# Kernel tuning notes

Hardware: AMD Instinct MI355X
Metric: run time of the kernel (lower is better)

Reference implementation:

```python
import jax, jax.numpy as jnp
import numpy as np
from jax import lax

EPS = 1e-5

def setup_inputs() -> dict:
    key = jax.random.key(0)
    k1, k2, k3, k4, k5, k6 = jax.random.split(key, 6)
    x = jax.random.normal(k1, (1, 64, 31, 96, 96), dtype=jnp.float32)
    # small init scale keeps gate pre-activations in a sane range
    w = jax.random.normal(k2, (256, 64, 3, 3, 3), dtype=jnp.float32) * 0.05
    gamma = jax.random.uniform(k3, (256,), dtype=jnp.float32)
    beta = jax.random.normal(k4, (256,), dtype=jnp.float32) * 0.1
    mean = jax.random.normal(k5, (256,), dtype=jnp.float32) * 0.1
    var = jax.random.uniform(k6, (256,), dtype=jnp.float32) + 0.5
    return {"x": x, "w": w, "gamma": gamma, "beta": beta, "mean": mean, "var": var}

def _bcast(p):
    return p[None, :, None, None, None]

def reference(x, w, gamma, beta, mean, var):
    # Conv3d (bias=False), stride 1, padding 1, NCDHW
    gates = lax.conv_general_dilated(
        x, w, window_strides=(1, 1, 1), padding=[(1, 1)] * 3,
        dimension_numbers=("NCDHW", "OIDHW", "NCDHW"))
    # BatchNorm3d (inference, running stats)
    scale = gamma * lax.rsqrt(var + EPS)
    gates = gates * _bcast(scale) + _bcast(beta - mean * scale)
    C = 64  # out_channels
    Wx = jnp.tanh(gates[:, 0 * C:1 * C])
    ft = jax.nn.sigmoid(gates[:, 1 * C:2 * C])
    rt = jax.nn.sigmoid(gates[:, 2 * C:3 * C])
    X = jnp.tanh(gates[:, 3 * C:4 * C])  # act == 'tanh'
    # time axis (dim 2) to front: (D, B, C, H, W)
    Wt = jnp.moveaxis(Wx, 2, 0)
    Ft = jnp.moveaxis(ft, 2, 0)
    Rt = jnp.moveaxis(rt, 2, 0)
    Xt = jnp.moveaxis(X, 2, 0)
    # t = 0: Ct = 1 - ft (note: Wx unused at first step, per source)
    C0 = 1.0 - Ft[0]
    h0 = Rt[0] * C0 + (1.0 - Rt[0]) * Xt[0]
    def step(Ct, inp):
        wx, f, r, xx = inp
        Ct = f * Ct + (1.0 - f) * wx
        ht = r * Ct + (1.0 - r) * xx
        return Ct, ht
    _, hs = lax.scan(step, C0, (Wt[1:], Ft[1:], Rt[1:], Xt[1:]))
    hts = jnp.concatenate([h0[None], hs], axis=0)  # (D,B,C,H,W)
    return jnp.moveaxis(hts, 0, 2)  # (B,C,D,H,W)
```

## Files before the change

kernel.cpp:

```cpp
#include <hip/hip_runtime.h>
#include <cstddef>

#define CI_  64
#define CO_  256
#define DD_  31
#define HH_  96
#define WW_  96
#define HW_  (HH_*WW_)
#define DHW_ (DD_*HW_)
#define EPSV 1e-5f

#define PD_   33
#define PH_   98
#define PW_   98
#define PHW_  9604
#define PDHW_ 316932

#define S_COL 8
#define S_CIG 144
#define S_ROW 1152
#define S_DD  11520
#define NTASK 4320
#define NTASKP 4352
#define XH_N  (NTASKP*8)

#define HTI_  12
#define WTI_  6
#define NTILE 72
#define NBLK  (NTILE*DD_)
#define GSP   128

typedef _Float16 half8   __attribute__((ext_vector_type(8)));
typedef _Float16 half4v  __attribute__((ext_vector_type(4)));
typedef _Float16 half2v  __attribute__((ext_vector_type(2)));
typedef float    float4v __attribute__((ext_vector_type(4)));

__device__ __forceinline__ void gl_lds16(const _Float16* g, _Float16* l) {
  __builtin_amdgcn_global_load_lds(
      (const __attribute__((address_space(1))) unsigned int*)(g),
      (__attribute__((address_space(3))) unsigned int*)(l), 16, 0, 0);
}

__global__ __launch_bounds__(256) void repack_w_k(const float* __restrict__ w,
                                                  _Float16* __restrict__ wr2) {
  int idx = blockIdx.x * 256 + threadIdx.x;
  if (idx >= 55296) return;
  int lw   = idx & 15;
  int quad = (idx >> 4) & 3;
  int cog  = (idx >> 6) & 15;
  int tkc  = idx >> 10;
  int kc   = tkc & 1;
  int t    = tkc >> 1;
  int co   = cog * 16 + lw;
  int cib  = kc * 32 + quad * 8;
  half8 v;
#pragma unroll
  for (int s = 0; s < 8; s++)
    v[s] = (_Float16)w[(size_t)co * 1728 + (size_t)(cib + s) * 27 + t];
  *(half8*)(wr2 + (size_t)idx * 8) = v;
}

__global__ __launch_bounds__(256) void transpose_x_k(const float* __restrict__ x,
                                                     _Float16* __restrict__ xt) {
  int p = blockIdx.x * 256 + threadIdx.x;
  if (p >= PDHW_) return;
  int pd  = p / PHW_;
  int rem = p - pd * PHW_;
  int ph  = rem / PW_;
  int pw  = rem - ph * PW_;
  bool in = (pd >= 1) & (pd <= DD_) & (ph >= 1) & (ph <= HH_) & (pw >= 1) & (pw <= WW_);
  if (in) {
    const float* xp = x + (size_t)(pd - 1) * HW_ + (size_t)(ph - 1) * WW_ + (pw - 1);
#pragma unroll
    for (int cig = 0; cig < 8; cig++) {
      half8 v;
#pragma unroll
      for (int s = 0; s < 8; s++)
        v[s] = (_Float16)xp[(size_t)(cig * 8 + s) * DHW_];
      *(half8*)(xt + ((size_t)cig * PDHW_ + p) * 8) = v;
    }
  } else {
    half8 z = (half8)(_Float16)0.f;
#pragma unroll
    for (int cig = 0; cig < 8; cig++)
      *(half8*)(xt + ((size_t)cig * PDHW_ + p) * 8) = z;
  }
}

__global__ __launch_bounds__(256, 2) void conv_mfma_k(
    const _Float16* __restrict__ xt, const _Float16* __restrict__ wr2,
    const float* __restrict__ gamma, const float* __restrict__ beta,
    const float* __restrict__ mean, const float* __restrict__ var,
    _Float16* __restrict__ gates)
{
  __shared__ _Float16 xh[XH_N];

  const int bid  = blockIdx.x;
  const int flat = (bid & 7) * 279 + (bid >> 3);
  const int d    = flat / NTILE;
  const int bx   = flat - d * NTILE;
  const int wti  = bx % 6;
  const int hti  = bx / 6;
  const int h0   = hti * 8, w0 = wti * 16;

  const int tid  = threadIdx.x;
  const int lane = tid & 63;
  const int wave = __builtin_amdgcn_readfirstlane(tid >> 6);
  const int lw   = lane & 15;
  const int quad = lane >> 4;

#pragma unroll 1
  for (int it = 0; it < 17; ++it) {
    const int wb   = it * 256 + wave * 64;
    const int task = wb + lane;
    const int tt   = task < NTASK ? task : (NTASK - 1);
    int col = tt % 18;
    int rc  = tt / 18;
    int cig = rc & 7;
    int dr  = rc >> 3;
    int dd  = dr / 10;
    int row = dr - dd * 10;
    const _Float16* g = xt + (((size_t)cig * PDHW_ + (size_t)(d + dd) * PHW_ +
                               (size_t)(h0 + row) * PW_ + (w0 + col)) << 3);
    gl_lds16(g, xh + (size_t)wb * 8);
  }

  float4v acc[8][4];
#pragma unroll
  for (int m = 0; m < 8; m++)
#pragma unroll
    for (int j = 0; j < 4; j++) acc[m][j] = (float4v)0.f;

  __syncthreads();

#pragma unroll 1
  for (int t9 = 0; t9 < 9; ++t9) {
    const int kd = t9 / 3;
    const int kh = t9 - kd * 3;
#pragma unroll
    for (int kc = 0; kc < 2; ++kc) {
#pragma unroll
      for (int kw = 0; kw < 3; ++kw) {
        const int t = t9 * 3 + kw;
        const _Float16* bp = wr2 + (((size_t)((t * 2 + kc) * 16 + wave * 4)) << 9) + (lane << 3);
        half8 bf[4];
#pragma unroll
        for (int j = 0; j < 4; ++j) bf[j] = *(const half8*)(bp + ((size_t)j << 9));
        const int ab = kd * S_DD + kh * S_ROW + (kc * 4 + quad) * S_CIG + (lw + kw) * S_COL;
#pragma unroll
        for (int m = 0; m < 8; ++m) {
          half8 af = *(const half8*)(xh + ab + m * S_ROW);
#pragma unroll
          for (int j = 0; j < 4; ++j)
            acc[m][j] = __builtin_amdgcn_mfma_f32_16x16x32_f16(af, bf[j], acc[m][j], 0, 0, 0);
        }
      }
    }
  }

  _Float16* gb = gates + ((size_t)(d * NTILE + bx) * 256) * GSP;
  const bool istanh = (wave == 0) || (wave == 3);
#pragma unroll
  for (int j = 0; j < 4; j++) {
    const int co = wave * 64 + j * 16 + lw;
    const float s  = gamma[co] * rsqrtf(var[co] + EPSV);
    const float bb = fmaf(-mean[co], s, beta[co]);
#pragma unroll
    for (int m = 0; m < 8; m++) {
      half4v hv;
#pragma unroll
      for (int reg = 0; reg < 4; reg++) {
        float v = fmaf(acc[m][j][reg], s, bb);
        float a;
        if (istanh) {
          float tt = __expf(-2.f * fabsf(v));
          float r  = (1.f - tt) * __builtin_amdgcn_rcpf(1.f + tt);
          a = copysignf(r, v);
        } else {
          a = __builtin_amdgcn_rcpf(1.f + __expf(-v));
        }
        hv[reg] = (_Float16)a;
      }
      *(half4v*)(gb + (size_t)co * GSP + m * 16 + quad * 4) = hv;
    }
  }
}

__global__ __launch_bounds__(256) void recurrence_k(const _Float16* __restrict__ gates,
                                                    float* __restrict__ out) {
  const int idx = blockIdx.x * 256 + threadIdx.x;
  const int ml2 = idx & 63;
  const int t2  = idx >> 6;
  const int c   = t2 / NTILE;
  const int bx  = t2 - c * NTILE;
  const int hti = bx / 6, wti = bx - hti * 6;
  const int sp  = ml2 * 2;
  const int h   = hti * 8 + (sp >> 4);
  const int w   = wti * 16 + (sp & 15);

  const size_t DSTR = (size_t)NTILE * 256 * GSP;
  const _Float16* g0 = gates + (size_t)bx * 256 * GSP + sp;
  float* op = out + (size_t)c * DHW_ + (size_t)h * WW_ + w;

#define LD(dv, gate) (*(const half2v*)(g0 + (size_t)(dv) * DSTR + (size_t)(c + ((gate) << 6)) * GSP))

  half2v cf = LD(0, 1), cr = LD(0, 2), cx = LD(0, 3);
  half2v nwx = LD(1, 0), nf = LD(1, 1), nr = LD(1, 2), nx = LD(1, 3);
  float C0 = 1.f - (float)cf[0];
  float C1 = 1.f - (float)cf[1];
  {
    float r0 = (float)cr[0], x0 = (float)cx[0];
    float r1 = (float)cr[1], x1 = (float)cx[1];
    float2 st = {fmaf(r0, C0 - x0, x0), fmaf(r1, C1 - x1, x1)};
    *(float2*)op = st;
  }
#pragma unroll 1
  for (int d = 1; d < DD_; d++) {
    half2v cwx = nwx; cf = nf; cr = nr; cx = nx;
    if (d < DD_ - 1) {
      nwx = LD(d + 1, 0); nf = LD(d + 1, 1);
      nr  = LD(d + 1, 2); nx = LD(d + 1, 3);
    }
    float wx0 = (float)cwx[0], f0 = (float)cf[0], r0 = (float)cr[0], x0 = (float)cx[0];
    float wx1 = (float)cwx[1], f1 = (float)cf[1], r1 = (float)cr[1], x1 = (float)cx[1];
    C0 = fmaf(f0, C0 - wx0, wx0);
    C1 = fmaf(f1, C1 - wx1, wx1);
    float2 st = {fmaf(r0, C0 - x0, x0), fmaf(r1, C1 - x1, x1)};
    *(float2*)(op + (size_t)d * HW_) = st;
  }
#undef LD
}

extern "C" void kernel_launch(void* const* d_in, const int* in_sizes, int n_in,
                              void* d_out, int out_size, void* d_ws, size_t ws_size,
                              hipStream_t stream) {
  const float* x     = (const float*)d_in[0];
  const float* w     = (const float*)d_in[1];
  const float* gamma = (const float*)d_in[2];
  const float* beta  = (const float*)d_in[3];
  const float* mean  = (const float*)d_in[4];
  const float* var   = (const float*)d_in[5];
  float* out = (float*)d_out;

  _Float16* wr2   = (_Float16*)d_ws;
  _Float16* xt    = (_Float16*)((char*)d_ws + 884736);
  _Float16* gates = (_Float16*)((char*)d_ws + 884736 + 40567296);

  repack_w_k<<<216, 256, 0, stream>>>(w, wr2);
  transpose_x_k<<<(PDHW_ + 255) / 256, 256, 0, stream>>>(x, xt);
  conv_mfma_k<<<NBLK, 256, 0, stream>>>(xt, wr2, gamma, beta, mean, var, gates);
  recurrence_k<<<(64 * NTILE * 64) / 256, 256, 0, stream>>>(gates, out);
}
```

Baseline: 412.2 us.

## Split conv waves 2x4 over M/N, vectorize transpose and recurrence

The conv kernel now runs 512 threads as eight waves in a 2x4 grid over spatial rows and output-channel groups. Each wave holds half the accumulators (4x4 instead of 8x4), which lowers register pressure and raises occupancy, at the cost of each wave loading the same weight fragments. The input transpose is split into a separate kernel that zeroes the padding and a float4-vectorized interior transpose. The recurrence now processes 4 pixels per thread with half4 loads and float4 stores.

```diff
diff --git a/kernel.cpp b/kernel.cpp
--- a/kernel.cpp
+++ b/kernel.cpp
@@ -24,15 +24,12 @@
 #define NTASKP 4352
 #define XH_N  (NTASKP*8)
 
-#define HTI_  12
-#define WTI_  6
 #define NTILE 72
 #define NBLK  (NTILE*DD_)
 #define GSP   128
 
 typedef _Float16 half8   __attribute__((ext_vector_type(8)));
 typedef _Float16 half4v  __attribute__((ext_vector_type(4)));
-typedef _Float16 half2v  __attribute__((ext_vector_type(2)));
 typedef float    float4v __attribute__((ext_vector_type(4)));
 
 __device__ __forceinline__ void gl_lds16(const _Float16* g, _Float16* l) {
@@ -60,8 +57,7 @@
   *(half8*)(wr2 + (size_t)idx * 8) = v;
 }
 
-__global__ __launch_bounds__(256) void transpose_x_k(const float* __restrict__ x,
-                                                     _Float16* __restrict__ xt) {
+__global__ __launch_bounds__(256) void pad_zero_k(_Float16* __restrict__ xt) {
   int p = blockIdx.x * 256 + threadIdx.x;
   if (p >= PDHW_) return;
   int pd  = p / PHW_;
@@ -69,25 +65,40 @@
   int ph  = rem / PW_;
   int pw  = rem - ph * PW_;
   bool in = (pd >= 1) & (pd <= DD_) & (ph >= 1) & (ph <= HH_) & (pw >= 1) & (pw <= WW_);
-  if (in) {
-    const float* xp = x + (size_t)(pd - 1) * HW_ + (size_t)(ph - 1) * WW_ + (pw - 1);
-#pragma unroll
-    for (int cig = 0; cig < 8; cig++) {
-      half8 v;
-#pragma unroll
-      for (int s = 0; s < 8; s++)
-        v[s] = (_Float16)xp[(size_t)(cig * 8 + s) * DHW_];
-      *(half8*)(xt + ((size_t)cig * PDHW_ + p) * 8) = v;
-    }
-  } else {
-    half8 z = (half8)(_Float16)0.f;
-#pragma unroll
-    for (int cig = 0; cig < 8; cig++)
-      *(half8*)(xt + ((size_t)cig * PDHW_ + p) * 8) = z;
-  }
-}
-
-__global__ __launch_bounds__(256, 2) void conv_mfma_k(
+  if (in) return;
+  half8 z = (half8)(_Float16)0.f;
+#pragma unroll
+  for (int cig = 0; cig < 8; cig++)
+    *(half8*)(xt + ((size_t)cig * PDHW_ + p) * 8) = z;
+}
+
+__global__ __launch_bounds__(256) void transpose_x_k(const float* __restrict__ x,
+                                                     _Float16* __restrict__ xt) {
+  int idx = blockIdx.x * 256 + threadIdx.x;
+  if (idx >= 31 * 96 * 24) return;
+  int wq  = idx % 24;
+  int rem = idx / 24;
+  int h   = rem % 96;
+  int d   = rem / 96;
+  const float* xp = x + (size_t)d * HW_ + (size_t)h * WW_ + wq * 4;
+  size_t p0 = (size_t)(d + 1) * PHW_ + (size_t)(h + 1) * PW_ + (wq * 4 + 1);
+#pragma unroll 1
+  for (int cig = 0; cig < 8; cig++) {
+    float4 vv[8];
+#pragma unroll
+    for (int s = 0; s < 8; s++)
+      vv[s] = *(const float4*)(xp + (size_t)(cig * 8 + s) * DHW_);
+#pragma unroll
+    for (int k = 0; k < 4; k++) {
+      half8 o;
+#pragma unroll
+      for (int s = 0; s < 8; s++) o[s] = (_Float16)(&vv[s].x)[k];
+      *(half8*)(xt + ((size_t)cig * PDHW_ + p0 + k) * 8) = o;
+    }
+  }
+}
+
+__global__ __launch_bounds__(512, 4) void conv_mfma_k(
     const _Float16* __restrict__ xt, const _Float16* __restrict__ wr2,
     const float* __restrict__ gamma, const float* __restrict__ beta,
     const float* __restrict__ mean, const float* __restrict__ var,
@@ -106,33 +117,38 @@
   const int tid  = threadIdx.x;
   const int lane = tid & 63;
   const int wave = __builtin_amdgcn_readfirstlane(tid >> 6);
+  const int wm   = wave >> 2;
+  const int wn   = wave & 3;
   const int lw   = lane & 15;
   const int quad = lane >> 4;
 
 #pragma unroll 1
-  for (int it = 0; it < 17; ++it) {
-    const int wb   = it * 256 + wave * 64;
-    const int task = wb + lane;
-    const int tt   = task < NTASK ? task : (NTASK - 1);
-    int col = tt % 18;
-    int rc  = tt / 18;
-    int cig = rc & 7;
-    int dr  = rc >> 3;
-    int dd  = dr / 10;
-    int row = dr - dd * 10;
-    const _Float16* g = xt + (((size_t)cig * PDHW_ + (size_t)(d + dd) * PHW_ +
-                               (size_t)(h0 + row) * PW_ + (w0 + col)) << 3);
-    gl_lds16(g, xh + (size_t)wb * 8);
-  }
-
-  float4v acc[8][4];
-#pragma unroll
-  for (int m = 0; m < 8; m++)
+  for (int it = 0; it < 9; ++it) {
+    const int wb = it * 512 + wave * 64;
+    if (wb < NTASKP) {
+      const int task = wb + lane;
+      const int tt   = task < NTASK ? task : (NTASK - 1);
+      int col = tt % 18;
+      int rc  = tt / 18;
+      int cig = rc & 7;
+      int dr  = rc >> 3;
+      int dd  = dr / 10;
+      int row = dr - dd * 10;
+      const _Float16* g = xt + (((size_t)cig * PDHW_ + (size_t)(d + dd) * PHW_ +
+                                 (size_t)(h0 + row) * PW_ + (w0 + col)) << 3);
+      gl_lds16(g, xh + (size_t)wb * 8);
+    }
+  }
+
+  float4v acc[4][4];
+#pragma unroll
+  for (int m = 0; m < 4; m++)
 #pragma unroll
     for (int j = 0; j < 4; j++) acc[m][j] = (float4v)0.f;
 
   __syncthreads();
 
+  const int abase0 = quad * S_CIG + lw * S_COL + (wm * 4) * S_ROW;
 #pragma unroll 1
   for (int t9 = 0; t9 < 9; ++t9) {
     const int kd = t9 / 3;
@@ -142,13 +158,13 @@
 #pragma unroll
       for (int kw = 0; kw < 3; ++kw) {
         const int t = t9 * 3 + kw;
-        const _Float16* bp = wr2 + (((size_t)((t * 2 + kc) * 16 + wave * 4)) << 9) + (lane << 3);
+        const _Float16* bp = wr2 + (((size_t)((t * 2 + kc) * 16 + wn * 4)) << 9) + (lane << 3);
         half8 bf[4];
 #pragma unroll
         for (int j = 0; j < 4; ++j) bf[j] = *(const half8*)(bp + ((size_t)j << 9));
-        const int ab = kd * S_DD + kh * S_ROW + (kc * 4 + quad) * S_CIG + (lw + kw) * S_COL;
-#pragma unroll
-        for (int m = 0; m < 8; ++m) {
+        const int ab = abase0 + kd * S_DD + kh * S_ROW + (kc * 4) * S_CIG + kw * S_COL;
+#pragma unroll
+        for (int m = 0; m < 4; ++m) {
           half8 af = *(const half8*)(xh + ab + m * S_ROW);
 #pragma unroll
           for (int j = 0; j < 4; ++j)
@@ -159,14 +175,14 @@
   }
 
   _Float16* gb = gates + ((size_t)(d * NTILE + bx) * 256) * GSP;
-  const bool istanh = (wave == 0) || (wave == 3);
+  const bool istanh = (wn == 0) || (wn == 3);
 #pragma unroll
   for (int j = 0; j < 4; j++) {
-    const int co = wave * 64 + j * 16 + lw;
+    const int co = wn * 64 + j * 16 + lw;
     const float s  = gamma[co] * rsqrtf(var[co] + EPSV);
     const float bb = fmaf(-mean[co], s, beta[co]);
 #pragma unroll
-    for (int m = 0; m < 8; m++) {
+    for (int m = 0; m < 4; m++) {
       half4v hv;
 #pragma unroll
       for (int reg = 0; reg < 4; reg++) {
@@ -181,7 +197,7 @@
         }
         hv[reg] = (_Float16)a;
       }
-      *(half4v*)(gb + (size_t)co * GSP + m * 16 + quad * 4) = hv;
+      *(half4v*)(gb + (size_t)co * GSP + (wm * 4 + m) * 16 + quad * 4) = hv;
     }
   }
 }
@@ -189,12 +205,12 @@
 __global__ __launch_bounds__(256) void recurrence_k(const _Float16* __restrict__ gates,
                                                     float* __restrict__ out) {
   const int idx = blockIdx.x * 256 + threadIdx.x;
-  const int ml2 = idx & 63;
-  const int t2  = idx >> 6;
+  const int q   = idx & 31;
+  const int t2  = idx >> 5;
   const int c   = t2 / NTILE;
   const int bx  = t2 - c * NTILE;
   const int hti = bx / 6, wti = bx - hti * 6;
-  const int sp  = ml2 * 2;
+  const int sp  = q * 4;
   const int h   = hti * 8 + (sp >> 4);
   const int w   = wti * 16 + (sp & 15);
 
@@ -202,31 +218,36 @@
   const _Float16* g0 = gates + (size_t)bx * 256 * GSP + sp;
   float* op = out + (size_t)c * DHW_ + (size_t)h * WW_ + w;
 
-#define LD(dv, gate) (*(const half2v*)(g0 + (size_t)(dv) * DSTR + (size_t)(c + ((gate) << 6)) * GSP))
-
-  half2v cf = LD(0, 1), cr = LD(0, 2), cx = LD(0, 3);
-  half2v nwx = LD(1, 0), nf = LD(1, 1), nr = LD(1, 2), nx = LD(1, 3);
-  float C0 = 1.f - (float)cf[0];
-  float C1 = 1.f - (float)cf[1];
+#define LD(dv, gate) (*(const half4v*)(g0 + (size_t)(dv) * DSTR + (size_t)(c + ((gate) << 6)) * GSP))
+
+  half4v cf = LD(0, 1), cr = LD(0, 2), cx = LD(0, 3);
+  half4v nwx = LD(1, 0), nf = LD(1, 1), nr = LD(1, 2), nx = LD(1, 3);
+  float C[4];
   {
-    float r0 = (float)cr[0], x0 = (float)cx[0];
-    float r1 = (float)cr[1], x1 = (float)cx[1];
-    float2 st = {fmaf(r0, C0 - x0, x0), fmaf(r1, C1 - x1, x1)};
-    *(float2*)op = st;
+    float4 st;
+#pragma unroll
+    for (int k = 0; k < 4; k++) {
+      C[k] = 1.f - (float)cf[k];
+      float r0 = (float)cr[k], x0 = (float)cx[k];
+      (&st.x)[k] = fmaf(r0, C[k] - x0, x0);
+    }
+    *(float4*)op = st;
   }
 #pragma unroll 1
   for (int d = 1; d < DD_; d++) {
-    half2v cwx = nwx; cf = nf; cr = nr; cx = nx;
+    half4v cwx = nwx; cf = nf; cr = nr; cx = nx;
     if (d < DD_ - 1) {
       nwx = LD(d + 1, 0); nf = LD(d + 1, 1);
       nr  = LD(d + 1, 2); nx = LD(d + 1, 3);
     }
-    float wx0 = (float)cwx[0], f0 = (float)cf[0], r0 = (float)cr[0], x0 = (float)cx[0];
-    float wx1 = (float)cwx[1], f1 = (float)cf[1], r1 = (float)cr[1], x1 = (float)cx[1];
-    C0 = fmaf(f0, C0 - wx0, wx0);
-    C1 = fmaf(f1, C1 - wx1, wx1);
-    float2 st = {fmaf(r0, C0 - x0, x0), fmaf(r1, C1 - x1, x1)};
-    *(float2*)(op + (size_t)d * HW_) = st;
+    float4 st;
+#pragma unroll
+    for (int k = 0; k < 4; k++) {
+      float wx0 = (float)cwx[k], f0 = (float)cf[k], r0 = (float)cr[k], x0 = (float)cx[k];
+      C[k] = fmaf(f0, C[k] - wx0, wx0);
+      (&st.x)[k] = fmaf(r0, C[k] - x0, x0);
+    }
+    *(float4*)(op + (size_t)d * HW_) = st;
   }
 #undef LD
 }
@@ -247,7 +268,8 @@
   _Float16* gates = (_Float16*)((char*)d_ws + 884736 + 40567296);
 
   repack_w_k<<<216, 256, 0, stream>>>(w, wr2);
-  transpose_x_k<<<(PDHW_ + 255) / 256, 256, 0, stream>>>(x, xt);
-  conv_mfma_k<<<NBLK, 256, 0, stream>>>(xt, wr2, gamma, beta, mean, var, gates);
-  recurrence_k<<<(64 * NTILE * 64) / 256, 256, 0, stream>>>(gates, out);
-}
+  pad_zero_k<<<(PDHW_ + 255) / 256, 256, 0, stream>>>(xt);
+  transpose_x_k<<<(31 * 96 * 24 + 255) / 256, 256, 0, stream>>>(x, xt);
+  conv_mfma_k<<<NBLK, 512, 0, stream>>>(xt, wr2, gamma, beta, mean, var, gates);
+  recurrence_k<<<(64 * NTILE * 32) / 256, 256, 0, stream>>>(gates, out);
+}
```

Measured after the change: 421.9 us. 2.3% more time.
